# Performance work log

Measured on AMD Instinct MI355X. Metric: run time of the kernel, lower is better.

## Reference

```python
import jax, jax.numpy as jnp
import numpy as np

N_NODES = 100000
N_EDGES = 3200000
D_IN = 256
D_OUT = 256


def setup_inputs() -> dict:
    key = jax.random.key(0)
    k1, k2, k3, k4, k5, k6 = jax.random.split(key, 6)
    x = jax.random.normal(k1, (N_NODES, D_IN), dtype=jnp.float32)
    edge_row = jax.random.randint(k2, (N_EDGES,), 0, N_NODES, dtype=jnp.int32)
    edge_col = jax.random.randint(k3, (N_EDGES,), 0, N_NODES, dtype=jnp.int32)
    edge_val = jax.random.uniform(k4, (N_EDGES,), dtype=jnp.float32)
    # nn.Linear(in_features, out_features): weight [out, in], bias [out]
    bound = 1.0 / np.sqrt(D_IN)
    W = jax.random.uniform(k5, (D_OUT, D_IN), minval=-bound, maxval=bound, dtype=jnp.float32)
    b = jax.random.uniform(k6, (D_OUT,), minval=-bound, maxval=bound, dtype=jnp.float32)
    return {"x": x, "edge_row": edge_row, "edge_col": edge_col, "edge_val": edge_val, "W": W, "b": b}


def reference(x, edge_row, edge_col, edge_val, W, b):
    # torch.sparse.mm(adj, x): for each edge (r, c, v): agg[r] += v * x[c]
    gathered = edge_val[:, None] * x[edge_col]              # [E, D_IN]
    agg = jax.ops.segment_sum(gathered, edge_row, num_segments=N_NODES)  # [N, D_IN]
    # nn.Linear: agg @ W.T + b
    return jnp.einsum('nd,od->no', agg, W) + b
```

## Files before the change

### kernel.cpp

```cpp
#include <hip/hip_runtime.h>
#include <cstdint>
#include <cstddef>

#define D 256
#define NPB 32
#define BROWS 512
#define NBUCK 196
#define CHUNK_E 4096

typedef __attribute__((ext_vector_type(8))) short short8;
typedef __attribute__((ext_vector_type(4))) float floatx4;

__device__ __forceinline__ unsigned short f2bf(float f) {
    union { float f; unsigned int u; } cv; cv.f = f;
    unsigned int u = cv.u;
    unsigned int r = (u + 0x7fffu + ((u >> 16) & 1u)) >> 16;
    return (unsigned short)r;
}

__device__ __forceinline__ float bf2f(unsigned short s) {
    union { unsigned int u; float f; } cv;
    cv.u = ((unsigned int)s) << 16;
    return cv.f;
}

__global__ void k_prep(const int* __restrict__ erow, int* __restrict__ blkbins,
                       const float* __restrict__ x, unsigned short* __restrict__ xb,
                       const float* __restrict__ W, unsigned short* __restrict__ Wp,
                       int e, int n) {
    __shared__ int lb[NBUCK];
    const int tid = threadIdx.x;
    if (tid < NBUCK) lb[tid] = 0;
    __syncthreads();
    int gid = blockIdx.x * blockDim.x + tid;
    if (gid < e) atomicAdd(&lb[erow[gid] >> 9], 1);
    size_t i = (size_t)gid * 8;
    if (i < (size_t)n * D) {
        float4 a = *(const float4*)&x[i];
        float4 b = *(const float4*)&x[i + 4];
        short8 v;
        v[0] = (short)f2bf(a.x); v[1] = (short)f2bf(a.y);
        v[2] = (short)f2bf(a.z); v[3] = (short)f2bf(a.w);
        v[4] = (short)f2bf(b.x); v[5] = (short)f2bf(b.y);
        v[6] = (short)f2bf(b.z); v[7] = (short)f2bf(b.w);
        *(short8*)&xb[i] = v;
    }
    if (gid < 8192) {
        int ct = gid >> 9, rem = gid & 511;
        int ks = rem >> 6, ln = rem & 63;
        int q = ln >> 4, l = ln & 15;
        const float* src = &W[(size_t)(ct * 16 + l) * D + ks * 32 + q * 8];
        float4 c = *(const float4*)src;
        float4 d2 = *(const float4*)(src + 4);
        short8 w;
        w[0] = (short)f2bf(c.x); w[1] = (short)f2bf(c.y);
        w[2] = (short)f2bf(c.z); w[3] = (short)f2bf(c.w);
        w[4] = (short)f2bf(d2.x); w[5] = (short)f2bf(d2.y);
        w[6] = (short)f2bf(d2.z); w[7] = (short)f2bf(d2.w);
        *(short8*)&Wp[(size_t)gid * 8] = w;
    }
    __syncthreads();
    if (tid < NBUCK && lb[tid])
        atomicAdd(&blkbins[(blockIdx.x >> 4) * NBUCK + tid], lb[tid]);
}

__global__ __launch_bounds__(256) void k_off(
    const int* __restrict__ blkbins, int* __restrict__ blkoff,
    int* __restrict__ btot, int nchunk) {
    __shared__ int sd[256];
    const int tid = threadIdx.x;
    const int bk = blockIdx.x;
    int carry = 0;
    for (int c0 = 0; c0 < nchunk; c0 += 256) {
        int c = c0 + tid;
        int v = (c < nchunk) ? blkbins[c * NBUCK + bk] : 0;
        sd[tid] = v;
        __syncthreads();
        for (int off = 1; off < 256; off <<= 1) {
            int t = (tid >= off) ? sd[tid - off] : 0;
            __syncthreads();
            sd[tid] += t;
            __syncthreads();
        }
        if (c < nchunk) blkoff[c * NBUCK + bk] = carry + sd[tid] - v;
        int tot = sd[255];
        __syncthreads();
        carry += tot;
    }
    if (tid == 0) btot[bk] = carry;
}

__global__ void k_bscan(const int* __restrict__ btot, int* __restrict__ bstart,
                        int* __restrict__ row_start, int n) {
    __shared__ int sd[256];
    const int tid = threadIdx.x;
    int v = (tid < NBUCK) ? btot[tid] : 0;
    sd[tid] = v;
    __syncthreads();
    for (int off = 1; off < 256; off <<= 1) {
        int t = (tid >= off) ? sd[tid - off] : 0;
        __syncthreads();
        sd[tid] += t;
        __syncthreads();
    }
    if (tid < NBUCK) bstart[tid] = sd[tid] - v;
    if (tid == 255) {
        bstart[NBUCK] = sd[255];
        row_start[n] = sd[255];
    }
}

__global__ __launch_bounds__(256) void k_stage(
    const int* __restrict__ erow, const int* __restrict__ ecol,
    const float* __restrict__ eval, const int* __restrict__ blkoff,
    const int* __restrict__ bstart, int2* __restrict__ staged, int e) {
    __shared__ int lb[NBUCK];
    __shared__ int gb[NBUCK];
    __shared__ int sc[256];
    __shared__ unsigned char bid[CHUNK_E];
    __shared__ int2 ebuf[CHUNK_E];
    const int tid = threadIdx.x;
    if (tid < NBUCK) lb[tid] = 0;
    __syncthreads();
    const int ebase = blockIdx.x * CHUNK_E;
    int bk[16], rk[16];
#pragma unroll
    for (int i = 0; i < 16; ++i) {
        int idx = ebase + i * 256 + tid;
        bk[i] = -1;
        if (idx < e) {
            bk[i] = erow[idx] >> 9;
            rk[i] = atomicAdd(&lb[bk[i]], 1);
        }
    }
    __syncthreads();
    int v = (tid < NBUCK) ? lb[tid] : 0;
    sc[tid] = v;
    __syncthreads();
    for (int off = 1; off < 256; off <<= 1) {
        int t = (tid >= off) ? sc[tid - off] : 0;
        __syncthreads();
        sc[tid] += t;
        __syncthreads();
    }
    int loff = sc[tid] - v;
    if (tid < NBUCK) {
        lb[tid] = loff;
        gb[tid] = bstart[tid] + blkoff[blockIdx.x * NBUCK + tid] - loff;
    }
    __syncthreads();
#pragma unroll
    for (int i = 0; i < 16; ++i) {
        if (bk[i] >= 0) {
            int idx = ebase + i * 256 + tid;
            int slot = lb[bk[i]] + rk[i];
            int r = erow[idx];
            ebuf[slot] = make_int2(((r & (BROWS - 1)) << 17) | ecol[idx],
                                   __float_as_int(eval[idx]));
            bid[slot] = (unsigned char)bk[i];
        }
    }
    __syncthreads();
    const int cnt = min(e - ebase, CHUNK_E);
#pragma unroll
    for (int i = 0; i < 16; ++i) {
        int s = i * 256 + tid;
        if (s < cnt) staged[gb[bid[s]] + s] = ebuf[s];
    }
}

__global__ __launch_bounds__(256) void k_csr(
    const int2* __restrict__ staged, const int* __restrict__ bstart,
    int* __restrict__ row_start, int* __restrict__ counts,
    int* __restrict__ dhist, int2* __restrict__ sedge, int n) {
    __shared__ int h[BROWS];
    __shared__ int sc[256];
    __shared__ int dh[256];
    const int b = blockIdx.x, tid = threadIdx.x;
    const int r0 = b * BROWS;
    h[tid] = 0; h[tid + 256] = 0; dh[tid] = 0;
    __syncthreads();
    const int beg = bstart[b];
    const int end = bstart[b + 1];
    for (int idx = beg + tid; idx < end; idx += 256) {
        int lr = ((unsigned)staged[idx].x) >> 17;
        atomicAdd(&h[lr], 1);
    }
    __syncthreads();
    int a0 = h[tid], a1 = h[tid + 256];
    sc[tid] = a0;
    __syncthreads();
    for (int off = 1; off < 256; off <<= 1) {
        int t = (tid >= off) ? sc[tid - off] : 0;
        __syncthreads();
        sc[tid] += t;
        __syncthreads();
    }
    int incl0 = sc[tid];
    int tot0 = sc[255];
    __syncthreads();
    sc[tid] = a1;
    __syncthreads();
    for (int off = 1; off < 256; off <<= 1) {
        int t = (tid >= off) ? sc[tid - off] : 0;
        __syncthreads();
        sc[tid] += t;
        __syncthreads();
    }
    int incl1 = sc[tid];
    __syncthreads();
    int cur0 = beg + incl0 - a0;
    int cur1 = beg + tot0 + incl1 - a1;
    h[tid] = cur0;
    h[tid + 256] = cur1;
    if (r0 + tid < n) {
        row_start[r0 + tid] = cur0;
        counts[r0 + tid] = a0;
        atomicAdd(&dh[255 - min(a0, 255)], 1);
    }
    if (r0 + 256 + tid < n) {
        row_start[r0 + 256 + tid] = cur1;
        counts[r0 + 256 + tid] = a1;
        atomicAdd(&dh[255 - min(a1, 255)], 1);
    }
    __syncthreads();
    if (dh[tid]) atomicAdd(&dhist[tid], dh[tid]);
    for (int idx = beg + tid; idx < end; idx += 256) {
        int2 sv = staged[idx];
        int lr = ((unsigned)sv.x) >> 17;
        int p = atomicAdd(&h[lr], 1);
        sedge[p] = make_int2(sv.x & 0x1FFFF, sv.y);
    }
}

__global__ __launch_bounds__(256) void k_perm(
    const int* __restrict__ counts, const int* __restrict__ dhist,
    int* __restrict__ dcur, int* __restrict__ perm, int n) {
    __shared__ int st[256];
    __shared__ int lh[256];
    __shared__ int lbase[256];
    const int tid = threadIdx.x;
    lh[tid] = 0;
    int dv = dhist[tid];
    st[tid] = dv;
    __syncthreads();
    for (int off = 1; off < 256; off <<= 1) {
        int t = (tid >= off) ? st[tid - off] : 0;
        __syncthreads();
        st[tid] += t;
        __syncthreads();
    }
    int start = st[tid] - dv;
    const int base = blockIdx.x * 2048 + tid * 8;
    int bkt[8], rank[8];
#pragma unroll
    for (int i = 0; i < 8; ++i) {
        int idx = base + i;
        if (idx < n) {
            bkt[i] = 255 - min(counts[idx], 255);
            rank[i] = atomicAdd(&lh[bkt[i]], 1);
        }
    }
    __syncthreads();
    if (lh[tid]) lbase[tid] = start + atomicAdd(&dcur[tid], lh[tid]);
    __syncthreads();
#pragma unroll
    for (int i = 0; i < 8; ++i) {
        int idx = base + i;
        if (idx < n) perm[lbase[bkt[i]] + rank[i]] = idx;
    }
}

__global__ __launch_bounds__(256) void k_gg(
    const unsigned short* __restrict__ xb, const int2* __restrict__ sedge,
    const int* __restrict__ row_start, const int* __restrict__ perm,
    const unsigned short* __restrict__ Wp, const float* __restrict__ bias,
    float* __restrict__ out, int n) {
    __shared__ __align__(16) unsigned short aggl[32][264];
    __shared__ int pnl[32];
    const int tid = threadIdx.x;
    const int lane = tid & 63;
    const int wv = tid >> 6;
    const int base = blockIdx.x * NPB + wv * 8;

    int pn[8], ebeg[8], eend[8];
    int maxd = 0;
#pragma unroll
    for (int j = 0; j < 8; ++j) {
        pn[j] = perm[min(base + j, n - 1)];
        ebeg[j] = row_start[pn[j]];
        eend[j] = row_start[pn[j] + 1];
        maxd = max(maxd, eend[j] - ebeg[j]);
    }
    if (lane == 0) {
#pragma unroll
        for (int j = 0; j < 8; ++j) pnl[wv * 8 + j] = pn[j];
    }
    float4 acc[8];
#pragma unroll
    for (int j = 0; j < 8; ++j) acc[j] = make_float4(0.f, 0.f, 0.f, 0.f);

    for (int it = 0; it < maxd; ++it) {
        int2 ev[8];
        ushort4 xv[8];
#pragma unroll
        for (int j = 0; j < 8; ++j) {
            int e = ebeg[j] + it;
            int ec = max(min(e, eend[j] - 1), 0);
            ev[j] = sedge[ec];
        }
#pragma unroll
        for (int j = 0; j < 8; ++j) {
            xv[j] = *(const ushort4*)&xb[(size_t)ev[j].x * D + lane * 4];
        }
#pragma unroll
        for (int j = 0; j < 8; ++j) {
            float v = (ebeg[j] + it < eend[j]) ? __int_as_float(ev[j].y) : 0.f;
            acc[j].x += v * bf2f(xv[j].x);
            acc[j].y += v * bf2f(xv[j].y);
            acc[j].z += v * bf2f(xv[j].z);
            acc[j].w += v * bf2f(xv[j].w);
        }
    }
#pragma unroll
    for (int j = 0; j < 8; ++j) {
        ushort4 u;
        u.x = f2bf(acc[j].x);
        u.y = f2bf(acc[j].y);
        u.z = f2bf(acc[j].z);
        u.w = f2bf(acc[j].w);
        *(ushort4*)&aggl[wv * 8 + j][lane * 4] = u;
    }
    __syncthreads();

    const int q = lane >> 4, l = lane & 15;
    const int rt = wv >> 1;
    const int cb = (wv & 1) * 8;
    floatx4 gac[8];
#pragma unroll
    for (int i = 0; i < 8; ++i) gac[i] = (floatx4){0.f, 0.f, 0.f, 0.f};
#pragma unroll
    for (int ks = 0; ks < 8; ++ks) {
        short8 a = *(const short8*)&aggl[rt * 16 + l][ks * 32 + q * 8];
#pragma unroll
        for (int i = 0; i < 8; ++i) {
            short8 b = *(const short8*)&Wp[(size_t)(((cb + i) * 8 + ks) * 64 + lane) * 8];
            gac[i] = __builtin_amdgcn_mfma_f32_16x16x32_bf16(a, b, gac[i], 0, 0, 0);
        }
    }
#pragma unroll
    for (int i = 0; i < 8; ++i) {
        int o = (cb + i) * 16 + l;
        float bv = bias[o];
#pragma unroll
        for (int r = 0; r < 4; ++r) {
            int row = rt * 16 + q * 4 + r;
            if (base - wv * 8 + row < n)
                out[(size_t)pnl[row] * D + o] = gac[i][r] + bv;
        }
    }
}

extern "C" void kernel_launch(void* const* d_in, const int* in_sizes, int n_in,
                              void* d_out, int out_size, void* d_ws, size_t ws_size,
                              hipStream_t stream) {
    const float* x    = (const float*)d_in[0];
    const int*   erow = (const int*)d_in[1];
    const int*   ecol = (const int*)d_in[2];
    const float* eval = (const float*)d_in[3];
    const float* W    = (const float*)d_in[4];
    const float* bias = (const float*)d_in[5];
    float* out = (float*)d_out;

    const int n = in_sizes[0] / D;
    const int e = in_sizes[1];
    const int nchunk = (e + CHUNK_E - 1) / CHUNK_E;

    int* blkbins   = (int*)d_ws;
    int* dhist     = blkbins + (size_t)nchunk * NBUCK;
    int* dcur      = dhist + 256;
    int* btot      = dcur + 256;
    int* bstart    = btot + NBUCK;
    int* counts    = bstart + NBUCK + 1;
    int* row_start = counts + n;
    int* perm      = row_start + n + 1;
    int* blkoff    = perm + n;
    int2* staged   = (int2*)(((uintptr_t)(blkoff + (size_t)nchunk * NBUCK) + 15) & ~(uintptr_t)15);
    int2* sedge    = staged + e;
    unsigned short* Wp = (unsigned short*)(sedge + e);
    unsigned short* xb = Wp + 65536;

    hipMemsetAsync(blkbins, 0, ((size_t)nchunk * NBUCK + 512) * sizeof(int), stream);

    k_prep<<<12500, 256, 0, stream>>>(erow, blkbins, x, xb, W, Wp, e, n);
    k_off<<<NBUCK, 256, 0, stream>>>(blkbins, blkoff, btot, nchunk);
    k_bscan<<<1, 256, 0, stream>>>(btot, bstart, row_start, n);
    k_stage<<<nchunk, 256, 0, stream>>>(erow, ecol, eval, blkoff, bstart, staged, e);
    k_csr<<<NBUCK, 256, 0, stream>>>(staged, bstart, row_start, counts, dhist, sedge, n);
    k_perm<<<49, 256, 0, stream>>>(counts, dhist, dcur, perm, n);
    k_gg<<<(n + NPB - 1) / NPB, 256, 0, stream>>>(xb, sedge, row_start, perm,
                                                  Wp, bias, out, n);
}
```

Measured before the change: 614.8 us.

## Sort edges within each row by column bucket for gather locality

The CSR build now does a two-pass counting sort per row-bucket. It first scatters edges by column block, then stably by row, so edges inside each row end up ordered by source-node region and the x gathers in the aggregation kernel get better cache locality. The binning in k_prep also moves to one block per 4096-edge chunk that writes its counts directly, replacing shared atomics into global bins plus a large memset. The cost is an extra read/write pass over the edge array in k_csr and fewer blocks doing the histogram work.

```diff
diff --git a/kernel.cpp b/kernel.cpp
--- a/kernel.cpp
+++ b/kernel.cpp
@@ -27,23 +27,31 @@
 __global__ void k_prep(const int* __restrict__ erow, int* __restrict__ blkbins,
                        const float* __restrict__ x, unsigned short* __restrict__ xb,
                        const float* __restrict__ W, unsigned short* __restrict__ Wp,
-                       int e, int n) {
+                       int e, int n, int nchunk) {
     __shared__ int lb[NBUCK];
     const int tid = threadIdx.x;
-    if (tid < NBUCK) lb[tid] = 0;
-    __syncthreads();
+    const bool bin_duty = ((int)blockIdx.x < nchunk);
+    if (bin_duty) {
+        if (tid < NBUCK) lb[tid] = 0;
+        __syncthreads();
+        const int ebase = blockIdx.x * CHUNK_E;
+#pragma unroll
+        for (int i = 0; i < 16; ++i) {
+            int idx = ebase + i * 256 + tid;
+            if (idx < e) atomicAdd(&lb[erow[idx] >> 9], 1);
+        }
+    }
     int gid = blockIdx.x * blockDim.x + tid;
-    if (gid < e) atomicAdd(&lb[erow[gid] >> 9], 1);
-    size_t i = (size_t)gid * 8;
-    if (i < (size_t)n * D) {
-        float4 a = *(const float4*)&x[i];
-        float4 b = *(const float4*)&x[i + 4];
+    size_t i8 = (size_t)gid * 8;
+    if (i8 < (size_t)n * D) {
+        float4 a = *(const float4*)&x[i8];
+        float4 b = *(const float4*)&x[i8 + 4];
         short8 v;
         v[0] = (short)f2bf(a.x); v[1] = (short)f2bf(a.y);
         v[2] = (short)f2bf(a.z); v[3] = (short)f2bf(a.w);
         v[4] = (short)f2bf(b.x); v[5] = (short)f2bf(b.y);
         v[6] = (short)f2bf(b.z); v[7] = (short)f2bf(b.w);
-        *(short8*)&xb[i] = v;
+        *(short8*)&xb[i8] = v;
     }
     if (gid < 8192) {
         int ct = gid >> 9, rem = gid & 511;
@@ -59,9 +67,10 @@
         w[6] = (short)f2bf(d2.z); w[7] = (short)f2bf(d2.w);
         *(short8*)&Wp[(size_t)gid * 8] = w;
     }
-    __syncthreads();
-    if (tid < NBUCK && lb[tid])
-        atomicAdd(&blkbins[(blockIdx.x >> 4) * NBUCK + tid], lb[tid]);
+    if (bin_duty) {
+        __syncthreads();
+        if (tid < NBUCK) blkbins[blockIdx.x * NBUCK + tid] = lb[tid];
+    }
 }
 
 __global__ __launch_bounds__(256) void k_off(
@@ -113,7 +122,7 @@
 __global__ __launch_bounds__(256) void k_stage(
     const int* __restrict__ erow, const int* __restrict__ ecol,
     const float* __restrict__ eval, const int* __restrict__ blkoff,
-    const int* __restrict__ bstart, int2* __restrict__ staged, int e) {
+    const int* __restrict__ bstart, int2* __restrict__ bufA, int e) {
     __shared__ int lb[NBUCK];
     __shared__ int gb[NBUCK];
     __shared__ int sc[256];
@@ -165,29 +174,31 @@
 #pragma unroll
     for (int i = 0; i < 16; ++i) {
         int s = i * 256 + tid;
-        if (s < cnt) staged[gb[bid[s]] + s] = ebuf[s];
+        if (s < cnt) bufA[gb[bid[s]] + s] = ebuf[s];
     }
 }
 
 __global__ __launch_bounds__(256) void k_csr(
-    const int2* __restrict__ staged, const int* __restrict__ bstart,
-    int* __restrict__ row_start, int* __restrict__ counts,
-    int* __restrict__ dhist, int2* __restrict__ sedge, int n) {
+    int2* __restrict__ bufA, int2* __restrict__ bufB,
+    const int* __restrict__ bstart, int* __restrict__ row_start,
+    int* __restrict__ counts, int* __restrict__ dhist, int n) {
     __shared__ int h[BROWS];
+    __shared__ int ch[256];
     __shared__ int sc[256];
     __shared__ int dh[256];
     const int b = blockIdx.x, tid = threadIdx.x;
     const int r0 = b * BROWS;
-    h[tid] = 0; h[tid + 256] = 0; dh[tid] = 0;
+    h[tid] = 0; h[tid + 256] = 0; dh[tid] = 0; ch[tid] = 0;
     __syncthreads();
     const int beg = bstart[b];
     const int end = bstart[b + 1];
     for (int idx = beg + tid; idx < end; idx += 256) {
-        int lr = ((unsigned)staged[idx].x) >> 17;
-        atomicAdd(&h[lr], 1);
-    }
-    __syncthreads();
-    int a0 = h[tid], a1 = h[tid + 256];
+        int sx = bufA[idx].x;
+        atomicAdd(&h[((unsigned)sx) >> 17], 1);
+        atomicAdd(&ch[(sx & 0x1FFFF) >> 9], 1);
+    }
+    __syncthreads();
+    int a0 = h[tid], a1 = h[tid + 256], c0 = ch[tid];
     sc[tid] = a0;
     __syncthreads();
     for (int off = 1; off < 256; off <<= 1) {
@@ -208,11 +219,22 @@
         __syncthreads();
     }
     int incl1 = sc[tid];
+    __syncthreads();
+    sc[tid] = c0;
+    __syncthreads();
+    for (int off = 1; off < 256; off <<= 1) {
+        int t = (tid >= off) ? sc[tid - off] : 0;
+        __syncthreads();
+        sc[tid] += t;
+        __syncthreads();
+    }
+    int inclc = sc[tid];
     __syncthreads();
     int cur0 = beg + incl0 - a0;
     int cur1 = beg + tot0 + incl1 - a1;
     h[tid] = cur0;
     h[tid + 256] = cur1;
+    ch[tid] = beg + inclc - c0;
     if (r0 + tid < n) {
         row_start[r0 + tid] = cur0;
         counts[r0 + tid] = a0;
@@ -226,10 +248,15 @@
     __syncthreads();
     if (dh[tid]) atomicAdd(&dhist[tid], dh[tid]);
     for (int idx = beg + tid; idx < end; idx += 256) {
-        int2 sv = staged[idx];
-        int lr = ((unsigned)sv.x) >> 17;
-        int p = atomicAdd(&h[lr], 1);
-        sedge[p] = make_int2(sv.x & 0x1FFFF, sv.y);
+        int2 sv = bufA[idx];
+        int p = atomicAdd(&ch[(sv.x & 0x1FFFF) >> 9], 1);
+        bufB[p] = sv;
+    }
+    __syncthreads();
+    for (int idx = beg + tid; idx < end; idx += 256) {
+        int2 sv = bufB[idx];
+        int p = atomicAdd(&h[((unsigned)sv.x) >> 17], 1);
+        bufA[p] = make_int2(sv.x & 0x1FFFF, sv.y);
     }
 }
 
@@ -376,28 +403,28 @@
     const int e = in_sizes[1];
     const int nchunk = (e + CHUNK_E - 1) / CHUNK_E;
 
-    int* blkbins   = (int*)d_ws;
-    int* dhist     = blkbins + (size_t)nchunk * NBUCK;
+    int* dhist     = (int*)d_ws;
     int* dcur      = dhist + 256;
     int* btot      = dcur + 256;
     int* bstart    = btot + NBUCK;
     int* counts    = bstart + NBUCK + 1;
     int* row_start = counts + n;
     int* perm      = row_start + n + 1;
-    int* blkoff    = perm + n;
-    int2* staged   = (int2*)(((uintptr_t)(blkoff + (size_t)nchunk * NBUCK) + 15) & ~(uintptr_t)15);
-    int2* sedge    = staged + e;
-    unsigned short* Wp = (unsigned short*)(sedge + e);
+    int* blkbins   = perm + n;
+    int* blkoff    = blkbins + (size_t)nchunk * NBUCK;
+    int2* bufA     = (int2*)(((uintptr_t)(blkoff + (size_t)nchunk * NBUCK) + 15) & ~(uintptr_t)15);
+    int2* bufB     = bufA + e;
+    unsigned short* Wp = (unsigned short*)(bufB + e);
     unsigned short* xb = Wp + 65536;
 
-    hipMemsetAsync(blkbins, 0, ((size_t)nchunk * NBUCK + 512) * sizeof(int), stream);
-
-    k_prep<<<12500, 256, 0, stream>>>(erow, blkbins, x, xb, W, Wp, e, n);
+    hipMemsetAsync(dhist, 0, 512 * sizeof(int), stream);
+
+    k_prep<<<12500, 256, 0, stream>>>(erow, blkbins, x, xb, W, Wp, e, n, nchunk);
     k_off<<<NBUCK, 256, 0, stream>>>(blkbins, blkoff, btot, nchunk);
     k_bscan<<<1, 256, 0, stream>>>(btot, bstart, row_start, n);
-    k_stage<<<nchunk, 256, 0, stream>>>(erow, ecol, eval, blkoff, bstart, staged, e);
-    k_csr<<<NBUCK, 256, 0, stream>>>(staged, bstart, row_start, counts, dhist, sedge, n);
+    k_stage<<<nchunk, 256, 0, stream>>>(erow, ecol, eval, blkoff, bstart, bufA, e);
+    k_csr<<<NBUCK, 256, 0, stream>>>(bufA, bufB, bstart, row_start, counts, dhist, n);
     k_perm<<<49, 256, 0, stream>>>(counts, dhist, dcur, perm, n);
-    k_gg<<<(n + NPB - 1) / NPB, 256, 0, stream>>>(xb, sedge, row_start, perm,
+    k_gg<<<(n + NPB - 1) / NPB, 256, 0, stream>>>(xb, bufA, row_start, perm,
                                                   Wp, bias, out, n);
 }
```

Measured after the change: 608.9 us. No clear change (-1.0%).
